# Optimization experiments

Measured on AMD Instinct MI355X. Metric: run time of the kernel, lower is better.

The kernel has to match this reference:

```python
import jax, jax.numpy as jnp
import numpy as np

# irreps '32x0e + 32x1o + 16x2e': dims 32 (l=0), 96 (l=1, 32x3), 80 (l=2, 16x5) -> 208
MUL0, MUL1, MUL2 = 32, 32, 16
SC = 64  # scalar_channels
N_NODES, N_EDGES = 50000, 200000
FAN_IN = MUL0 * MUL0 + MUL1 * MUL1 + MUL2 * MUL2  # fully-connected path fan-in


def setup_inputs() -> dict:
    key = jax.random.key(0)
    ks = jax.random.split(key, 10)
    node_tensors = jax.random.normal(ks[0], (N_NODES, 208), dtype=jnp.float32)
    edge_index = jax.random.randint(ks[1], (2, N_EDGES), 0, N_NODES)
    # FullyConnectedTensorProduct path weights (mul1, mul2, mul_out)
    W0 = jax.random.normal(ks[2], (MUL0, MUL0, SC), dtype=jnp.float32)
    W1 = jax.random.normal(ks[3], (MUL1, MUL1, SC), dtype=jnp.float32)
    W2 = jax.random.normal(ks[4], (MUL2, MUL2, SC), dtype=jnp.float32)
    # MLP: Linear(64,32) -> SiLU -> Linear(32,1)
    A1 = jax.random.normal(ks[5], (SC, SC // 2), dtype=jnp.float32) / np.float32(np.sqrt(SC))
    b1 = jnp.zeros((SC // 2,), dtype=jnp.float32)
    A2 = jax.random.normal(ks[6], (SC // 2, 1), dtype=jnp.float32) / np.float32(np.sqrt(SC // 2))
    b2 = jnp.zeros((1,), dtype=jnp.float32)
    return {"node_tensors": node_tensors, "edge_index": edge_index,
            "W0": W0, "W1": W1, "W2": W2, "A1": A1, "b1": b1, "A2": A2, "b2": b2}


def _split_irreps(x):
    # x: [E, 208] -> scalars [E,32], vectors [E,32,3], rank-2 [E,16,5]
    s = x[:, :MUL0]
    v = x[:, MUL0:MUL0 + MUL1 * 3].reshape(-1, MUL1, 3)
    t = x[:, MUL0 + MUL1 * 3:].reshape(-1, MUL2, 5)
    return s, v, t


def reference(node_tensors, edge_index, W0, W1, W2, A1, b1, A2, b2):
    src, dst = edge_index[0], edge_index[1]
    x1 = node_tensors[src]  # [E, 208]
    x2 = node_tensors[dst]
    s1, v1, t1 = _split_irreps(x1)
    s2, v2, t2 = _split_irreps(x2)
    alpha = np.float32(1.0 / np.sqrt(FAN_IN))  # path normalization
    # l x l -> 0 Clebsch-Gordan: delta_{m1 m2} / sqrt(2l+1)
    e = alpha * (
        jnp.einsum('eu,ev,uvw->ew', s1, s2, W0)
        + jnp.einsum('eum,evm,uvw->ew', v1, v2, W1) / np.float32(np.sqrt(3.0))
        + jnp.einsum('eum,evm,uvw->ew', t1, t2, W2) / np.float32(np.sqrt(5.0))
    )  # [E, 64]
    h = jax.nn.silu(e @ A1 + b1)
    return (h @ A2 + b2)[:, 0]  # [E]
```

## Files before the change

kernel.cpp:

```cpp
#include <hip/hip_runtime.h>
#include <hip/hip_fp16.h>
#include <stdint.h>

#define N_EDGES 200000
#define N_NODES 50000
#define BM 128
#define NT 512

typedef _Float16 f16x8 __attribute__((ext_vector_type(8)));
typedef float f32x4 __attribute__((ext_vector_type(4)));

__global__ void prep_w(const float* __restrict__ W0, const float* __restrict__ W1,
                       const float* __restrict__ W2, uint16_t* __restrict__ wt) {
  int o = blockIdx.x * 256 + threadIdx.x;
  int T = o >> 11, r = o & 2047, w = r >> 5, kk = r & 31;
  int k = T * 32 + kk;
  const float AS = 1.0f / 48.0f;
  const float AV = AS * 0.57735026918962576f;
  const float AT = AS * 0.44721359549995794f;
  float val;
  if (k < 1024)      val = AS * W0[(k >> 5) * 2048 + (k & 31) * 64 + w];
  else if (k < 2048) { int k2 = k - 1024; val = AV * W1[(k2 >> 5) * 2048 + (k2 & 31) * 64 + w]; }
  else               { int k2 = k - 2048; val = AT * W2[(k2 >> 4) * 1024 + (k2 & 15) * 64 + w]; }
  __half h = __float2half(val);
  wt[o] = *reinterpret_cast<uint16_t*>(&h);
}

__global__ void prep_tables(const float* __restrict__ nt,
                            uint16_t* __restrict__ ta, uint16_t* __restrict__ tb) {
  long long o = (long long)blockIdx.x * 256 + threadIdx.x;
  if (o >= (long long)N_NODES * 296) return;
  int node = (int)(o / 296);
  int r = (int)(o - (long long)node * 296);
  const float* x = nt + (size_t)node * 208;
  float va = 0.f;
  if (r < 32) va = x[r];
  else if (r < 160) { int q = r - 32;  int u = q >> 2, m = q & 3;  if (m < 3) va = x[32 + u * 3 + m]; }
  else if (r < 288) { int q = r - 160; int u = q >> 3, m = q & 7;  if (m < 5) va = x[128 + u * 5 + m]; }
  __half ha = __float2half(va);
  ta[(size_t)node * 296 + r] = *reinterpret_cast<uint16_t*>(&ha);
  if (r < 216) {
    float vb = 0.f;
    if (r < 32) vb = x[r];
    else if (r < 128) { int q = r - 32;  int m = q >> 5, v = q & 31; vb = x[32 + v * 3 + m]; }
    else if (r < 208) { int q = r - 128; int m = q >> 4, v = q & 15; vb = x[128 + v * 5 + m]; }
    __half hb = __float2half(vb);
    tb[(size_t)node * 216 + r] = *reinterpret_cast<uint16_t*>(&hb);
  }
}

__device__ __forceinline__ void gload16(const void* g, void* l) {
  __builtin_amdgcn_global_load_lds(
      (const __attribute__((address_space(1))) void*)g,
      (__attribute__((address_space(3))) void*)l, 16, 0, 0);
}

#define LOADW(WRA, TEXPR)                                                       \
  { int Tc_ = (TEXPR);                                                          \
    _Pragma("unroll") for (int nf = 0; nf < 4; ++nf)                            \
      WRA[nf] = wtg4[Tc_ * 256 + nf * 64 + lo4]; }

#define MSTEPA(WRA, A)                                                          \
  _Pragma("unroll") for (int mf = 0; mf < 2; ++mf)                              \
  _Pragma("unroll") for (int nf = 0; nf < 4; ++nf)                              \
    acc[mf][nf] = __builtin_amdgcn_mfma_f32_16x16x32_f16(                       \
        (A)[mf], *(const f16x8*)&WRA[nf], acc[mf][nf], 0, 0, 0);

#define BUILD_S(T_, A)                                                          \
  _Pragma("unroll") for (int mf = 0; mf < 2; ++mf) {                            \
    __half s1v = *(const __half*)(x1b[mf] + 2 * (T_));                          \
    __half2 s1b2 = __half2half2(s1v);                                           \
    union { uint32_t u[4]; f16x8 v; } au_;                                      \
    _Pragma("unroll") for (int q = 0; q < 4; ++q) {                             \
      __half2 p = __hmul2(s1b2, ((const __half2*)&s2pk[mf])[q]);                \
      au_.u[q] = *(uint32_t*)&p;                                                \
    }                                                                           \
    (A)[mf] = au_.v;                                                            \
  }

#define BUILD_V(U_, A)                                                          \
  _Pragma("unroll") for (int mf = 0; mf < 2; ++mf) {                            \
    uint2 vv_ = *(const uint2*)(x1b[mf] + 64 + (U_) * 8);                       \
    __half2 h01_ = *(__half2*)&vv_.x;                                           \
    __half2 h2x_ = *(__half2*)&vv_.y;                                           \
    __half2 va0 = __half2half2(__low2half(h01_));                               \
    __half2 va1 = __half2half2(__high2half(h01_));                              \
    __half2 va2 = __half2half2(__low2half(h2x_));                               \
    union { uint32_t u[4]; f16x8 v; } au_;                                      \
    _Pragma("unroll") for (int q = 0; q < 4; ++q) {                             \
      __half2 p = __hmul2(va0, ((const __half2*)&v2pk[mf][0])[q]);              \
      p = __hfma2(va1, ((const __half2*)&v2pk[mf][1])[q], p);                   \
      p = __hfma2(va2, ((const __half2*)&v2pk[mf][2])[q], p);                   \
      au_.u[q] = *(uint32_t*)&p;                                                \
    }                                                                           \
    (A)[mf] = au_.v;                                                            \
  }

#define BUILD_T(TT_, A)                                                         \
  _Pragma("unroll") for (int mm = 0; mm < 2; ++mm) {                            \
    int u_ = (TT_) * 2 + (g >> 1);                                              \
    uint4 tv_ = *(const uint4*)(x1b[mm] + 320 + u_ * 16);                       \
    __half2 w01_ = *(__half2*)&tv_.x;                                           \
    __half2 w23_ = *(__half2*)&tv_.y;                                           \
    __half2 w4x_ = *(__half2*)&tv_.z;                                           \
    __half2 tb0 = __half2half2(__low2half(w01_));                               \
    __half2 tb1 = __half2half2(__high2half(w01_));                              \
    __half2 tb2 = __half2half2(__low2half(w23_));                               \
    __half2 tb3 = __half2half2(__high2half(w23_));                              \
    __half2 tb4 = __half2half2(__low2half(w4x_));                               \
    union { uint32_t u[4]; f16x8 v; } au_;                                      \
    _Pragma("unroll") for (int q = 0; q < 4; ++q) {                             \
      __half2 p = __hmul2(tb0, ((const __half2*)&t2pk[mm][0])[q]);              \
      p = __hfma2(tb1, ((const __half2*)&t2pk[mm][1])[q], p);                   \
      p = __hfma2(tb2, ((const __half2*)&t2pk[mm][2])[q], p);                   \
      p = __hfma2(tb3, ((const __half2*)&t2pk[mm][3])[q], p);                   \
      p = __hfma2(tb4, ((const __half2*)&t2pk[mm][4])[q], p);                   \
      au_.u[q] = *(uint32_t*)&p;                                                \
    }                                                                           \
    (A)[mm] = au_.v;                                                            \
  }

#define RING_S(WRA, P, T0) { f16x8 a[2]; BUILD_S((T0) + (P), a); MSTEPA(WRA, a); LOADW(WRA, (T0) + (P) + 4); }
#define RING_V(WRA, P, T0) { f16x8 a[2]; BUILD_V((T0) + (P) - 32, a); MSTEPA(WRA, a); LOADW(WRA, (T0) + (P) + 4); }
#define WRAPT(X) ((X) <= 71 ? (X) : (X) - 8)
#define RING_T(WRA, P, T0) { f16x8 a[2]; BUILD_T((T0) + (P) - 64, a); MSTEPA(WRA, a); LOADW(WRA, WRAPT((T0) + (P) + 4)); }

__global__ __launch_bounds__(NT, 2) void edge_main(
    const uint16_t* __restrict__ ta, const uint16_t* __restrict__ tbl,
    const int* __restrict__ ei, const uint16_t* __restrict__ wt,
    const float* __restrict__ A1, const float* __restrict__ b1,
    const float* __restrict__ A2, const float* __restrict__ b2,
    float* __restrict__ out)
{
  __shared__ alignas(16) unsigned char smem[77824];
  const int tid = threadIdx.x;
  const int e0 = blockIdx.x * BM;

  {
    #pragma unroll
    for (int i = 0; i < 9; ++i) {
      unsigned idx = i * 512 + tid;
      unsigned row = idx / 37u;
      unsigned cj = idx - row * 37u;
      int e = e0 + (int)row; if (e > N_EDGES - 1) e = N_EDGES - 1;
      int src = ei[e];
      const char* gp = (const char*)ta + (size_t)src * 592 + cj * 16;
      void* lp = (void*)(smem + i * 8192 + (tid >> 6) * 1024);
      gload16(gp, lp);
    }
    if (tid < 128) {
      unsigned idx = 4608 + tid;
      unsigned row = idx / 37u;
      unsigned cj = idx - row * 37u;
      int e = e0 + (int)row; if (e > N_EDGES - 1) e = N_EDGES - 1;
      int src = ei[e];
      const char* gp = (const char*)ta + (size_t)src * 592 + cj * 16;
      void* lp = (void*)(smem + 73728 + (tid >> 6) * 1024);
      gload16(gp, lp);
    }
  }
  asm volatile("s_waitcnt vmcnt(0)" ::: "memory");
  __syncthreads();

  const int lane = tid & 63, c = lane & 15, g = lane >> 4;
  const int wv = tid >> 6;
  const int m = wv >> 1;
  const int kh = wv & 1;
  const int lo4 = c * 4 + g;

  const unsigned char* x1b[2];
  const unsigned char* tbp[2];
  #pragma unroll
  for (int mf = 0; mf < 2; ++mf) {
    int erow = m * 32 + mf * 16 + c;
    x1b[mf] = smem + (size_t)erow * 592;
    int e = e0 + erow; if (e > N_EDGES - 1) e = N_EDGES - 1;
    int dst = ei[N_EDGES + e];
    tbp[mf] = (const unsigned char*)tbl + (size_t)dst * 432;
  }

  f32x4 acc[2][4];
  #pragma unroll
  for (int mf = 0; mf < 2; ++mf)
    #pragma unroll
    for (int nf = 0; nf < 4; ++nf) acc[mf][nf] = (f32x4){0.f, 0.f, 0.f, 0.f};

  const uint4* wtg4 = (const uint4*)wt;
  uint4 wr0[4], wr1[4], wr2[4], wr3[4];

  if (kh == 0) {
    uint4 s2pk[2];
    #pragma unroll
    for (int mf = 0; mf < 2; ++mf) s2pk[mf] = *(const uint4*)(tbp[mf] + g * 16);
    LOADW(wr0, 0); LOADW(wr1, 1); LOADW(wr2, 2); LOADW(wr3, 3);
    for (int T = 0; T < 32; T += 4) {
      RING_S(wr0, 0, T); RING_S(wr1, 1, T); RING_S(wr2, 2, T); RING_S(wr3, 3, T);
    }
    uint4 v2pk[2][3];
    #pragma unroll
    for (int mf = 0; mf < 2; ++mf)
      #pragma unroll
      for (int m3 = 0; m3 < 3; ++m3)
        v2pk[mf][m3] = *(const uint4*)(tbp[mf] + 64 + m3 * 64 + g * 16);
    for (int T = 32; T < 44; T += 4) {
      RING_V(wr0, 0, T); RING_V(wr1, 1, T); RING_V(wr2, 2, T); RING_V(wr3, 3, T);
    }
  } else {
    uint4 v2pk[2][3];
    #pragma unroll
    for (int mf = 0; mf < 2; ++mf)
      #pragma unroll
      for (int m3 = 0; m3 < 3; ++m3)
        v2pk[mf][m3] = *(const uint4*)(tbp[mf] + 64 + m3 * 64 + g * 16);
    LOADW(wr0, 44); LOADW(wr1, 45); LOADW(wr2, 46); LOADW(wr3, 47);
    for (int T = 44; T < 64; T += 4) {
      RING_V(wr0, 0, T); RING_V(wr1, 1, T); RING_V(wr2, 2, T); RING_V(wr3, 3, T);
    }
    {
      uint4 t2pk[2][5];
      #pragma unroll
      for (int mm = 0; mm < 2; ++mm)
        #pragma unroll
        for (int m5 = 0; m5 < 5; ++m5)
          t2pk[mm][m5] = *(const uint4*)(tbp[mm] + 256 + m5 * 32 + (g & 1) * 16);
      RING_T(wr0, 0, 64); RING_T(wr1, 1, 64); RING_T(wr2, 2, 64); RING_T(wr3, 3, 64);
      RING_T(wr0, 0, 68); RING_T(wr1, 1, 68); RING_T(wr2, 2, 68); RING_T(wr3, 3, 68);
    }
  }

  __syncthreads();
  float* etile = (float*)smem;
  #pragma unroll
  for (int mf = 0; mf < 2; ++mf)
    #pragma unroll
    for (int nf = 0; nf < 4; ++nf)
      #pragma unroll
      for (int rr = 0; rr < 4; ++rr)
        etile[(size_t)(kh * 128 + m * 32 + mf * 16 + g * 4 + rr) * 68 + nf * 16 + c] =
            acc[mf][nf][rr];
  {
    float4* d4 = (float4*)(smem + 69632);
    d4[tid] = ((const float4*)A1)[tid];
  }
  __syncthreads();

  if (tid < 256) {
    int el = tid >> 1, jh = tid & 1;
    const float* er0 = etile + (size_t)el * 68;
    const float* er1 = etile + (size_t)(128 + el) * 68;
    const float* A1s = (const float*)(smem + 69632);
    float hacc[16];
    #pragma unroll
    for (int j = 0; j < 16; ++j) hacc[j] = b1[jh * 16 + j];
    for (int w4 = 0; w4 < 16; ++w4) {
      float4 ea = *(const float4*)(er0 + w4 * 4);
      float4 eb = *(const float4*)(er1 + w4 * 4);
      #pragma unroll
      for (int q2 = 0; q2 < 4; ++q2) {
        float ev = (&ea.x)[q2] + (&eb.x)[q2];
        int w = w4 * 4 + q2;
        float4 a0 = *(const float4*)(A1s + w * 32 + jh * 16);
        float4 a1 = *(const float4*)(A1s + w * 32 + jh * 16 + 4);
        float4 a2 = *(const float4*)(A1s + w * 32 + jh * 16 + 8);
        float4 a3 = *(const float4*)(A1s + w * 32 + jh * 16 + 12);
        hacc[0]  += ev * a0.x; hacc[1]  += ev * a0.y; hacc[2]  += ev * a0.z; hacc[3]  += ev * a0.w;
        hacc[4]  += ev * a1.x; hacc[5]  += ev * a1.y; hacc[6]  += ev * a1.z; hacc[7]  += ev * a1.w;
        hacc[8]  += ev * a2.x; hacc[9]  += ev * a2.y; hacc[10] += ev * a2.z; hacc[11] += ev * a2.w;
        hacc[12] += ev * a3.x; hacc[13] += ev * a3.y; hacc[14] += ev * a3.z; hacc[15] += ev * a3.w;
      }
    }
    float o = 0.f;
    #pragma unroll
    for (int j = 0; j < 16; ++j) {
      float z = hacc[j];
      o += (z / (1.f + __expf(-z))) * A2[jh * 16 + j];
    }
    o += __shfl_xor(o, 1);
    int e = e0 + el;
    if (jh == 0 && e < N_EDGES) out[e] = o + b2[0];
  }
}

extern "C" void kernel_launch(void* const* d_in, const int* in_sizes, int n_in,
                              void* d_out, int out_size, void* d_ws, size_t ws_size,
                              hipStream_t stream) {
  const float* nt = (const float*)d_in[0];
  const int*   ei = (const int*)d_in[1];
  const float* W0 = (const float*)d_in[2];
  const float* W1 = (const float*)d_in[3];
  const float* W2 = (const float*)d_in[4];
  const float* A1 = (const float*)d_in[5];
  const float* b1 = (const float*)d_in[6];
  const float* A2 = (const float*)d_in[7];
  const float* b2 = (const float*)d_in[8];
  float* out = (float*)d_out;

  uint16_t* wt = (uint16_t*)d_ws;
  uint16_t* ta = (uint16_t*)((char*)d_ws + 294912);
  uint16_t* tb = (uint16_t*)((char*)d_ws + 294912 + (size_t)N_NODES * 592);

  prep_w<<<576, 256, 0, stream>>>(W0, W1, W2, wt);
  {
    long long tot = (long long)N_NODES * 296;
    int blocks = (int)((tot + 255) / 256);
    prep_tables<<<blocks, 256, 0, stream>>>(nt, ta, tb);
  }
  edge_main<<<(N_EDGES + BM - 1) / BM, NT, 0, stream>>>(ta, tb, ei, wt, A1, b1, A2, b2, out);
}
```

Before: 202.2 us.

## Switch edge kernel to single-wave blocks of 32 edges with full K

```diff
diff --git a/kernel.cpp b/kernel.cpp
--- a/kernel.cpp
+++ b/kernel.cpp
@@ -4,8 +4,8 @@
 
 #define N_EDGES 200000
 #define N_NODES 50000
-#define BM 128
-#define NT 512
+#define BM 32
+#define NT 64
 
 typedef _Float16 f16x8 __attribute__((ext_vector_type(8)));
 typedef float f32x4 __attribute__((ext_vector_type(4)));
@@ -125,56 +125,50 @@
 #define WRAPT(X) ((X) <= 71 ? (X) : (X) - 8)
 #define RING_T(WRA, P, T0) { f16x8 a[2]; BUILD_T((T0) + (P) - 64, a); MSTEPA(WRA, a); LOADW(WRA, WRAPT((T0) + (P) + 4)); }
 
-__global__ __launch_bounds__(NT, 2) void edge_main(
+__global__ __launch_bounds__(NT) void edge_main(
     const uint16_t* __restrict__ ta, const uint16_t* __restrict__ tbl,
     const int* __restrict__ ei, const uint16_t* __restrict__ wt,
     const float* __restrict__ A1, const float* __restrict__ b1,
     const float* __restrict__ A2, const float* __restrict__ b2,
     float* __restrict__ out)
 {
-  __shared__ alignas(16) unsigned char smem[77824];
+  __shared__ alignas(16) unsigned char smem[18944];
   const int tid = threadIdx.x;
   const int e0 = blockIdx.x * BM;
 
   {
     #pragma unroll
-    for (int i = 0; i < 9; ++i) {
-      unsigned idx = i * 512 + tid;
+    for (int i = 0; i < 18; ++i) {
+      unsigned idx = i * 64 + tid;
       unsigned row = idx / 37u;
       unsigned cj = idx - row * 37u;
-      int e = e0 + (int)row; if (e > N_EDGES - 1) e = N_EDGES - 1;
+      int e = e0 + (int)row;
       int src = ei[e];
       const char* gp = (const char*)ta + (size_t)src * 592 + cj * 16;
-      void* lp = (void*)(smem + i * 8192 + (tid >> 6) * 1024);
-      gload16(gp, lp);
-    }
-    if (tid < 128) {
-      unsigned idx = 4608 + tid;
+      gload16(gp, (void*)(smem + i * 1024));
+    }
+    if (tid < 32) {
+      unsigned idx = 1152 + tid;
       unsigned row = idx / 37u;
       unsigned cj = idx - row * 37u;
-      int e = e0 + (int)row; if (e > N_EDGES - 1) e = N_EDGES - 1;
+      int e = e0 + (int)row;
       int src = ei[e];
       const char* gp = (const char*)ta + (size_t)src * 592 + cj * 16;
-      void* lp = (void*)(smem + 73728 + (tid >> 6) * 1024);
-      gload16(gp, lp);
+      gload16(gp, (void*)(smem + 18432));
     }
   }
   asm volatile("s_waitcnt vmcnt(0)" ::: "memory");
-  __syncthreads();
-
-  const int lane = tid & 63, c = lane & 15, g = lane >> 4;
-  const int wv = tid >> 6;
-  const int m = wv >> 1;
-  const int kh = wv & 1;
+
+  const int lane = tid, c = lane & 15, g = lane >> 4;
   const int lo4 = c * 4 + g;
 
   const unsigned char* x1b[2];
   const unsigned char* tbp[2];
   #pragma unroll
   for (int mf = 0; mf < 2; ++mf) {
-    int erow = m * 32 + mf * 16 + c;
+    int erow = mf * 16 + c;
     x1b[mf] = smem + (size_t)erow * 592;
-    int e = e0 + erow; if (e > N_EDGES - 1) e = N_EDGES - 1;
+    int e = e0 + erow;
     int dst = ei[N_EDGES + e];
     tbp[mf] = (const unsigned char*)tbl + (size_t)dst * 432;
   }
@@ -188,7 +182,7 @@
   const uint4* wtg4 = (const uint4*)wt;
   uint4 wr0[4], wr1[4], wr2[4], wr3[4];
 
-  if (kh == 0) {
+  {
     uint4 s2pk[2];
     #pragma unroll
     for (int mf = 0; mf < 2; ++mf) s2pk[mf] = *(const uint4*)(tbp[mf] + g * 16);
@@ -196,73 +190,54 @@
     for (int T = 0; T < 32; T += 4) {
       RING_S(wr0, 0, T); RING_S(wr1, 1, T); RING_S(wr2, 2, T); RING_S(wr3, 3, T);
     }
+  }
+  {
     uint4 v2pk[2][3];
     #pragma unroll
     for (int mf = 0; mf < 2; ++mf)
       #pragma unroll
       for (int m3 = 0; m3 < 3; ++m3)
         v2pk[mf][m3] = *(const uint4*)(tbp[mf] + 64 + m3 * 64 + g * 16);
-    for (int T = 32; T < 44; T += 4) {
+    for (int T = 32; T < 64; T += 4) {
       RING_V(wr0, 0, T); RING_V(wr1, 1, T); RING_V(wr2, 2, T); RING_V(wr3, 3, T);
     }
-  } else {
-    uint4 v2pk[2][3];
-    #pragma unroll
-    for (int mf = 0; mf < 2; ++mf)
-      #pragma unroll
-      for (int m3 = 0; m3 < 3; ++m3)
-        v2pk[mf][m3] = *(const uint4*)(tbp[mf] + 64 + m3 * 64 + g * 16);
-    LOADW(wr0, 44); LOADW(wr1, 45); LOADW(wr2, 46); LOADW(wr3, 47);
-    for (int T = 44; T < 64; T += 4) {
-      RING_V(wr0, 0, T); RING_V(wr1, 1, T); RING_V(wr2, 2, T); RING_V(wr3, 3, T);
-    }
-    {
-      uint4 t2pk[2][5];
-      #pragma unroll
-      for (int mm = 0; mm < 2; ++mm)
-        #pragma unroll
-        for (int m5 = 0; m5 < 5; ++m5)
-          t2pk[mm][m5] = *(const uint4*)(tbp[mm] + 256 + m5 * 32 + (g & 1) * 16);
-      RING_T(wr0, 0, 64); RING_T(wr1, 1, 64); RING_T(wr2, 2, 64); RING_T(wr3, 3, 64);
-      RING_T(wr0, 0, 68); RING_T(wr1, 1, 68); RING_T(wr2, 2, 68); RING_T(wr3, 3, 68);
-    }
-  }
-
-  __syncthreads();
-  float* etile = (float*)smem;
+  }
+  {
+    uint4 t2pk[2][5];
+    #pragma unroll
+    for (int mm = 0; mm < 2; ++mm)
+      #pragma unroll
+      for (int m5 = 0; m5 < 5; ++m5)
+        t2pk[mm][m5] = *(const uint4*)(tbp[mm] + 256 + m5 * 32 + (g & 1) * 16);
+    RING_T(wr0, 0, 64); RING_T(wr1, 1, 64); RING_T(wr2, 2, 64); RING_T(wr3, 3, 64);
+    RING_T(wr0, 0, 68); RING_T(wr1, 1, 68); RING_T(wr2, 2, 68); RING_T(wr3, 3, 68);
+  }
+
+  float* ew = (float*)smem;
   #pragma unroll
   for (int mf = 0; mf < 2; ++mf)
     #pragma unroll
     for (int nf = 0; nf < 4; ++nf)
       #pragma unroll
       for (int rr = 0; rr < 4; ++rr)
-        etile[(size_t)(kh * 128 + m * 32 + mf * 16 + g * 4 + rr) * 68 + nf * 16 + c] =
-            acc[mf][nf][rr];
-  {
-    float4* d4 = (float4*)(smem + 69632);
-    d4[tid] = ((const float4*)A1)[tid];
-  }
-  __syncthreads();
-
-  if (tid < 256) {
-    int el = tid >> 1, jh = tid & 1;
-    const float* er0 = etile + (size_t)el * 68;
-    const float* er1 = etile + (size_t)(128 + el) * 68;
-    const float* A1s = (const float*)(smem + 69632);
+        ew[(size_t)(mf * 16 + g * 4 + rr) * 68 + nf * 16 + c] = acc[mf][nf][rr];
+
+  {
+    int el = lane >> 1, jh = lane & 1;
+    const float* er = ew + (size_t)el * 68;
     float hacc[16];
     #pragma unroll
     for (int j = 0; j < 16; ++j) hacc[j] = b1[jh * 16 + j];
     for (int w4 = 0; w4 < 16; ++w4) {
-      float4 ea = *(const float4*)(er0 + w4 * 4);
-      float4 eb = *(const float4*)(er1 + w4 * 4);
+      float4 ea = *(const float4*)(er + w4 * 4);
       #pragma unroll
       for (int q2 = 0; q2 < 4; ++q2) {
-        float ev = (&ea.x)[q2] + (&eb.x)[q2];
+        float ev = (&ea.x)[q2];
         int w = w4 * 4 + q2;
-        float4 a0 = *(const float4*)(A1s + w * 32 + jh * 16);
-        float4 a1 = *(const float4*)(A1s + w * 32 + jh * 16 + 4);
-        float4 a2 = *(const float4*)(A1s + w * 32 + jh * 16 + 8);
-        float4 a3 = *(const float4*)(A1s + w * 32 + jh * 16 + 12);
+        float4 a0 = *(const float4*)(A1 + w * 32 + jh * 16);
+        float4 a1 = *(const float4*)(A1 + w * 32 + jh * 16 + 4);
+        float4 a2 = *(const float4*)(A1 + w * 32 + jh * 16 + 8);
+        float4 a3 = *(const float4*)(A1 + w * 32 + jh * 16 + 12);
         hacc[0]  += ev * a0.x; hacc[1]  += ev * a0.y; hacc[2]  += ev * a0.z; hacc[3]  += ev * a0.w;
         hacc[4]  += ev * a1.x; hacc[5]  += ev * a1.y; hacc[6]  += ev * a1.z; hacc[7]  += ev * a1.w;
         hacc[8]  += ev * a2.x; hacc[9]  += ev * a2.y; hacc[10] += ev * a2.z; hacc[11] += ev * a2.w;
@@ -305,5 +280,5 @@
     int blocks = (int)((tot + 255) / 256);
     prep_tables<<<blocks, 256, 0, stream>>>(nt, ta, tb);
   }
-  edge_main<<<(N_EDGES + BM - 1) / BM, NT, 0, stream>>>(ta, tb, ei, wt, A1, b1, A2, b2, out);
-}
+  edge_main<<<N_EDGES / BM, NT, 0, stream>>>(ta, tb, ei, wt, A1, b1, A2, b2, out);
+}
```

After: 221.0 us. +9.3%, slower.

## Process four edge subtiles per block with double-buffered async x1 gather

Applied to the files above, without the earlier changes.

```diff
diff --git a/kernel.cpp b/kernel.cpp
--- a/kernel.cpp
+++ b/kernel.cpp
@@ -4,7 +4,8 @@
 
 #define N_EDGES 200000
 #define N_NODES 50000
-#define BM 128
+#define BM 512
+#define SUB 128
 #define NT 512
 
 typedef _Float16 f16x8 __attribute__((ext_vector_type(8)));
@@ -125,6 +126,28 @@
 #define WRAPT(X) ((X) <= 71 ? (X) : (X) - 8)
 #define RING_T(WRA, P, T0) { f16x8 a[2]; BUILD_T((T0) + (P) - 64, a); MSTEPA(WRA, a); LOADW(WRA, WRAPT((T0) + (P) + 4)); }
 
+#define STAGE_X1(ST, BUFB)                                                      \
+  { int eb_ = e0 + (ST) * SUB;                                                  \
+    _Pragma("unroll") for (int i = 0; i < 9; ++i) {                             \
+      unsigned idx = i * 512u + tid;                                            \
+      unsigned row = idx / 37u;                                                 \
+      unsigned cj = idx - row * 37u;                                            \
+      int e = eb_ + (int)row; if (e > N_EDGES - 1) e = N_EDGES - 1;             \
+      int src = ei[e];                                                          \
+      gload16((const char*)ta + (size_t)src * 592 + cj * 16,                    \
+              (void*)((BUFB) + i * 8192 + (tid >> 6) * 1024));                  \
+    }                                                                           \
+    if (tid < 128) {                                                            \
+      unsigned idx = 4608 + tid;                                                \
+      unsigned row = idx / 37u;                                                 \
+      unsigned cj = idx - row * 37u;                                            \
+      int e = eb_ + (int)row; if (e > N_EDGES - 1) e = N_EDGES - 1;             \
+      int src = ei[e];                                                          \
+      gload16((const char*)ta + (size_t)src * 592 + cj * 16,                    \
+              (void*)((BUFB) + 73728 + (tid >> 6) * 1024));                     \
+    }                                                                           \
+  }
+
 __global__ __launch_bounds__(NT, 2) void edge_main(
     const uint16_t* __restrict__ ta, const uint16_t* __restrict__ tbl,
     const int* __restrict__ ei, const uint16_t* __restrict__ wt,
@@ -132,152 +155,134 @@
     const float* __restrict__ A2, const float* __restrict__ b2,
     float* __restrict__ out)
 {
-  __shared__ alignas(16) unsigned char smem[77824];
+  __shared__ alignas(16) unsigned char smem[151552];
   const int tid = threadIdx.x;
   const int e0 = blockIdx.x * BM;
-
-  {
-    #pragma unroll
-    for (int i = 0; i < 9; ++i) {
-      unsigned idx = i * 512 + tid;
-      unsigned row = idx / 37u;
-      unsigned cj = idx - row * 37u;
-      int e = e0 + (int)row; if (e > N_EDGES - 1) e = N_EDGES - 1;
-      int src = ei[e];
-      const char* gp = (const char*)ta + (size_t)src * 592 + cj * 16;
-      void* lp = (void*)(smem + i * 8192 + (tid >> 6) * 1024);
-      gload16(gp, lp);
-    }
-    if (tid < 128) {
-      unsigned idx = 4608 + tid;
-      unsigned row = idx / 37u;
-      unsigned cj = idx - row * 37u;
-      int e = e0 + (int)row; if (e > N_EDGES - 1) e = N_EDGES - 1;
-      int src = ei[e];
-      const char* gp = (const char*)ta + (size_t)src * 592 + cj * 16;
-      void* lp = (void*)(smem + 73728 + (tid >> 6) * 1024);
-      gload16(gp, lp);
-    }
-  }
-  asm volatile("s_waitcnt vmcnt(0)" ::: "memory");
-  __syncthreads();
-
   const int lane = tid & 63, c = lane & 15, g = lane >> 4;
   const int wv = tid >> 6;
   const int m = wv >> 1;
   const int kh = wv & 1;
   const int lo4 = c * 4 + g;
-
-  const unsigned char* x1b[2];
-  const unsigned char* tbp[2];
-  #pragma unroll
-  for (int mf = 0; mf < 2; ++mf) {
-    int erow = m * 32 + mf * 16 + c;
-    x1b[mf] = smem + (size_t)erow * 592;
-    int e = e0 + erow; if (e > N_EDGES - 1) e = N_EDGES - 1;
-    int dst = ei[N_EDGES + e];
-    tbp[mf] = (const unsigned char*)tbl + (size_t)dst * 432;
-  }
-
-  f32x4 acc[2][4];
-  #pragma unroll
-  for (int mf = 0; mf < 2; ++mf)
+  const uint4* wtg4 = (const uint4*)wt;
+
+  STAGE_X1(0, smem);
+  asm volatile("s_waitcnt vmcnt(0)" ::: "memory");
+  __syncthreads();
+  STAGE_X1(1, smem + 75776);
+
+  #pragma unroll 1
+  for (int st = 0; st < 4; ++st) {
+    unsigned char* bufb = (st & 1) ? (smem + 75776) : smem;
+
+    const unsigned char* x1b[2];
+    const unsigned char* tbp[2];
     #pragma unroll
-    for (int nf = 0; nf < 4; ++nf) acc[mf][nf] = (f32x4){0.f, 0.f, 0.f, 0.f};
-
-  const uint4* wtg4 = (const uint4*)wt;
-  uint4 wr0[4], wr1[4], wr2[4], wr3[4];
-
-  if (kh == 0) {
-    uint4 s2pk[2];
-    #pragma unroll
-    for (int mf = 0; mf < 2; ++mf) s2pk[mf] = *(const uint4*)(tbp[mf] + g * 16);
-    LOADW(wr0, 0); LOADW(wr1, 1); LOADW(wr2, 2); LOADW(wr3, 3);
-    for (int T = 0; T < 32; T += 4) {
-      RING_S(wr0, 0, T); RING_S(wr1, 1, T); RING_S(wr2, 2, T); RING_S(wr3, 3, T);
+    for (int mf = 0; mf < 2; ++mf) {
+      int erow = m * 32 + mf * 16 + c;
+      x1b[mf] = bufb + (size_t)erow * 592;
+      int e = e0 + st * SUB + erow; if (e > N_EDGES - 1) e = N_EDGES - 1;
+      int dst = ei[N_EDGES + e];
+      tbp[mf] = (const unsigned char*)tbl + (size_t)dst * 432;
     }
-    uint4 v2pk[2][3];
+
+    f32x4 acc[2][4];
     #pragma unroll
     for (int mf = 0; mf < 2; ++mf)
       #pragma unroll
-      for (int m3 = 0; m3 < 3; ++m3)
-        v2pk[mf][m3] = *(const uint4*)(tbp[mf] + 64 + m3 * 64 + g * 16);
-    for (int T = 32; T < 44; T += 4) {
-      RING_V(wr0, 0, T); RING_V(wr1, 1, T); RING_V(wr2, 2, T); RING_V(wr3, 3, T);
+      for (int nf = 0; nf < 4; ++nf) acc[mf][nf] = (f32x4){0.f, 0.f, 0.f, 0.f};
+
+    uint4 wr0[4], wr1[4], wr2[4], wr3[4];
+
+    if (kh == 0) {
+      uint4 s2pk[2];
+      #pragma unroll
+      for (int mf = 0; mf < 2; ++mf) s2pk[mf] = *(const uint4*)(tbp[mf] + g * 16);
+      LOADW(wr0, 0); LOADW(wr1, 1); LOADW(wr2, 2); LOADW(wr3, 3);
+      for (int T = 0; T < 32; T += 4) {
+        RING_S(wr0, 0, T); RING_S(wr1, 1, T); RING_S(wr2, 2, T); RING_S(wr3, 3, T);
+      }
+      uint4 v2pk[2][3];
+      #pragma unroll
+      for (int mf = 0; mf < 2; ++mf)
+        #pragma unroll
+        for (int m3 = 0; m3 < 3; ++m3)
+          v2pk[mf][m3] = *(const uint4*)(tbp[mf] + 64 + m3 * 64 + g * 16);
+      for (int T = 32; T < 44; T += 4) {
+        RING_V(wr0, 0, T); RING_V(wr1, 1, T); RING_V(wr2, 2, T); RING_V(wr3, 3, T);
+      }
+    } else {
+      uint4 v2pk[2][3];
+      #pragma unroll
+      for (int mf = 0; mf < 2; ++mf)
+        #pragma unroll
+        for (int m3 = 0; m3 < 3; ++m3)
+          v2pk[mf][m3] = *(const uint4*)(tbp[mf] + 64 + m3 * 64 + g * 16);
+      LOADW(wr0, 44); LOADW(wr1, 45); LOADW(wr2, 46); LOADW(wr3, 47);
+      for (int T = 44; T < 64; T += 4) {
+        RING_V(wr0, 0, T); RING_V(wr1, 1, T); RING_V(wr2, 2, T); RING_V(wr3, 3, T);
+      }
+      {
+        uint4 t2pk[2][5];
+        #pragma unroll
+        for (int mm = 0; mm < 2; ++mm)
+          #pragma unroll
+          for (int m5 = 0; m5 < 5; ++m5)
+            t2pk[mm][m5] = *(const uint4*)(tbp[mm] + 256 + m5 * 32 + (g & 1) * 16);
+        RING_T(wr0, 0, 64); RING_T(wr1, 1, 64); RING_T(wr2, 2, 64); RING_T(wr3, 3, 64);
+        RING_T(wr0, 0, 68); RING_T(wr1, 1, 68); RING_T(wr2, 2, 68); RING_T(wr3, 3, 68);
+      }
     }
-  } else {
-    uint4 v2pk[2][3];
+
+    __syncthreads();
+
+    float* etile = (float*)bufb;
     #pragma unroll
     for (int mf = 0; mf < 2; ++mf)
       #pragma unroll
-      for (int m3 = 0; m3 < 3; ++m3)
-        v2pk[mf][m3] = *(const uint4*)(tbp[mf] + 64 + m3 * 64 + g * 16);
-    LOADW(wr0, 44); LOADW(wr1, 45); LOADW(wr2, 46); LOADW(wr3, 47);
-    for (int T = 44; T < 64; T += 4) {
-      RING_V(wr0, 0, T); RING_V(wr1, 1, T); RING_V(wr2, 2, T); RING_V(wr3, 3, T);
+      for (int nf = 0; nf < 4; ++nf)
+        #pragma unroll
+        for (int rr = 0; rr < 4; ++rr)
+          etile[(size_t)(kh * 128 + m * 32 + mf * 16 + g * 4 + rr) * 68 + nf * 16 + c] =
+              acc[mf][nf][rr];
+    __syncthreads();
+
+    if (tid < 256) {
+      int el = tid >> 1, jh = tid & 1;
+      const float* er0 = etile + (size_t)el * 68;
+      const float* er1 = etile + (size_t)(128 + el) * 68;
+      float hacc[16];
+      #pragma unroll
+      for (int j = 0; j < 16; ++j) hacc[j] = b1[jh * 16 + j];
+      for (int w4 = 0; w4 < 16; ++w4) {
+        float4 ea = *(const float4*)(er0 + w4 * 4);
+        float4 eb = *(const float4*)(er1 + w4 * 4);
+        #pragma unroll
+        for (int q2 = 0; q2 < 4; ++q2) {
+          float ev = (&ea.x)[q2] + (&eb.x)[q2];
+          int w = w4 * 4 + q2;
+          float4 a0 = *(const float4*)(A1 + w * 32 + jh * 16);
+          float4 a1 = *(const float4*)(A1 + w * 32 + jh * 16 + 4);
+          float4 a2 = *(const float4*)(A1 + w * 32 + jh * 16 + 8);
+          float4 a3 = *(const float4*)(A1 + w * 32 + jh * 16 + 12);
+          hacc[0]  += ev * a0.x; hacc[1]  += ev * a0.y; hacc[2]  += ev * a0.z; hacc[3]  += ev * a0.w;
+          hacc[4]  += ev * a1.x; hacc[5]  += ev * a1.y; hacc[6]  += ev * a1.z; hacc[7]  += ev * a1.w;
+          hacc[8]  += ev * a2.x; hacc[9]  += ev * a2.y; hacc[10] += ev * a2.z; hacc[11] += ev * a2.w;
+          hacc[12] += ev * a3.x; hacc[13] += ev * a3.y; hacc[14] += ev * a3.z; hacc[15] += ev * a3.w;
+        }
+      }
+      float o = 0.f;
+      #pragma unroll
+      for (int j = 0; j < 16; ++j) {
+        float z = hacc[j];
+        o += (z / (1.f + __expf(-z))) * A2[jh * 16 + j];
+      }
+      o += __shfl_xor(o, 1);
+      int e = e0 + st * SUB + el;
+      if (jh == 0 && e < N_EDGES) out[e] = o + b2[0];
     }
-    {
-      uint4 t2pk[2][5];
-      #pragma unroll
-      for (int mm = 0; mm < 2; ++mm)
-        #pragma unroll
-        for (int m5 = 0; m5 < 5; ++m5)
-          t2pk[mm][m5] = *(const uint4*)(tbp[mm] + 256 + m5 * 32 + (g & 1) * 16);
-      RING_T(wr0, 0, 64); RING_T(wr1, 1, 64); RING_T(wr2, 2, 64); RING_T(wr3, 3, 64);
-      RING_T(wr0, 0, 68); RING_T(wr1, 1, 68); RING_T(wr2, 2, 68); RING_T(wr3, 3, 68);
-    }
-  }
-
-  __syncthreads();
-  float* etile = (float*)smem;
-  #pragma unroll
-  for (int mf = 0; mf < 2; ++mf)
-    #pragma unroll
-    for (int nf = 0; nf < 4; ++nf)
-      #pragma unroll
-      for (int rr = 0; rr < 4; ++rr)
-        etile[(size_t)(kh * 128 + m * 32 + mf * 16 + g * 4 + rr) * 68 + nf * 16 + c] =
-            acc[mf][nf][rr];
-  {
-    float4* d4 = (float4*)(smem + 69632);
-    d4[tid] = ((const float4*)A1)[tid];
-  }
-  __syncthreads();
-
-  if (tid < 256) {
-    int el = tid >> 1, jh = tid & 1;
-    const float* er0 = etile + (size_t)el * 68;
-    const float* er1 = etile + (size_t)(128 + el) * 68;
-    const float* A1s = (const float*)(smem + 69632);
-    float hacc[16];
-    #pragma unroll
-    for (int j = 0; j < 16; ++j) hacc[j] = b1[jh * 16 + j];
-    for (int w4 = 0; w4 < 16; ++w4) {
-      float4 ea = *(const float4*)(er0 + w4 * 4);
-      float4 eb = *(const float4*)(er1 + w4 * 4);
-      #pragma unroll
-      for (int q2 = 0; q2 < 4; ++q2) {
-        float ev = (&ea.x)[q2] + (&eb.x)[q2];
-        int w = w4 * 4 + q2;
-        float4 a0 = *(const float4*)(A1s + w * 32 + jh * 16);
-        float4 a1 = *(const float4*)(A1s + w * 32 + jh * 16 + 4);
-        float4 a2 = *(const float4*)(A1s + w * 32 + jh * 16 + 8);
-        float4 a3 = *(const float4*)(A1s + w * 32 + jh * 16 + 12);
-        hacc[0]  += ev * a0.x; hacc[1]  += ev * a0.y; hacc[2]  += ev * a0.z; hacc[3]  += ev * a0.w;
-        hacc[4]  += ev * a1.x; hacc[5]  += ev * a1.y; hacc[6]  += ev * a1.z; hacc[7]  += ev * a1.w;
-        hacc[8]  += ev * a2.x; hacc[9]  += ev * a2.y; hacc[10] += ev * a2.z; hacc[11] += ev * a2.w;
-        hacc[12] += ev * a3.x; hacc[13] += ev * a3.y; hacc[14] += ev * a3.z; hacc[15] += ev * a3.w;
-      }
-    }
-    float o = 0.f;
-    #pragma unroll
-    for (int j = 0; j < 16; ++j) {
-      float z = hacc[j];
-      o += (z / (1.f + __expf(-z))) * A2[jh * 16 + j];
-    }
-    o += __shfl_xor(o, 1);
-    int e = e0 + el;
-    if (jh == 0 && e < N_EDGES) out[e] = o + b2[0];
+    __syncthreads();
+
+    if (st + 2 < 4) { STAGE_X1(st + 2, bufb); }
   }
 }
 
```

After: 356.7 us. 76.4% more time.
